# Optimization experiments

Hardware: AMD Instinct MI355X
Metric: run time of the kernel (lower is better)

Reference implementation:

```python
import jax, jax.numpy as jnp
import numpy as np

B, TOPK, E, C, K = 64, 2, 16, 1024, 4096


def setup_inputs() -> dict:
    key = jax.random.key(0)
    k1, k2, k3, k4, k5, k6 = jax.random.split(key, 6)
    return {
        "activated": jax.random.normal(k1, (B, TOPK, K), dtype=jnp.float32),
        "expert_indices": jax.random.randint(k2, (B, TOPK), 0, E, dtype=jnp.int64)
        if jax.config.jax_enable_x64 else jax.random.randint(k2, (B, TOPK), 0, E, dtype=jnp.int32),
        "expert_weights": jax.random.uniform(k3, (B, TOPK), dtype=jnp.float32),
        "mlp2_weight": jax.random.normal(k4, (E, C, K), dtype=jnp.float32),
        "mlp2_bias": jax.random.normal(k5, (E, C), dtype=jnp.float32),
        "residual_x": jax.random.normal(k6, (B, C), dtype=jnp.float32),
    }


def reference(activated, expert_indices, expert_weights, mlp2_weight, mlp2_bias, residual_x):
    # Gather per-token expert weights/biases: w [B, topk, C, K], b [B, topk, C]
    w = mlp2_weight[expert_indices]
    b = mlp2_bias[expert_indices]
    # Batched matvec per (token, expert slot): t [B, topk, C]
    t = jnp.einsum("beck,bek->bec", w, activated) + b
    # Weighted combine over top-k expert slots, plus residual: [B, C]
    return residual_x + jnp.einsum("bec,be->bc", t, expert_weights)
```

## Files before the change

### kernel.cpp

```cpp
#include <hip/hip_runtime.h>

#define BB    64
#define TOPK  2
#define EE    16
#define CC    1024
#define KK    4096

constexpr int RPB = 8;
constexpr int P   = 16;
constexpr int KC  = 512;
constexpr int KC4 = KC / 4;

__global__ __launch_bounds__(256) void route_init(
    const int* __restrict__ idx, const float* __restrict__ ew,
    const float* __restrict__ bias, const float* __restrict__ resid,
    float* __restrict__ out, int* __restrict__ cnt, int* __restrict__ lists)
{
    if (blockIdx.x == 0) {
        __shared__ int scnt[EE];
        if (threadIdx.x < EE) scnt[threadIdx.x] = 0;
        __syncthreads();
        if (threadIdx.x < BB * TOPK) {
            int e = idx[threadIdx.x];
            int pos = atomicAdd(&scnt[e], 1);
            lists[e * 128 + pos] = threadIdx.x;
        }
        __syncthreads();
        if (threadIdx.x < EE) cnt[threadIdx.x] = scnt[threadIdx.x];
    } else {
        int i = (blockIdx.x - 1) * 256 + threadIdx.x;
        int b = i >> 10;
        int c = i & (CC - 1);
        float v = resid[i];
#pragma unroll
        for (int s = 0; s < TOPK; s++) {
            int e = idx[b * TOPK + s];
            v += ew[b * TOPK + s] * bias[e * CC + c];
        }
        out[i] = v;
    }
}

__global__ __launch_bounds__(256, 2) void moe_mlp2(
    const float* __restrict__ act, const float* __restrict__ ew,
    const float* __restrict__ W, float* __restrict__ out,
    const int* __restrict__ cnt, const int* __restrict__ lists)
{
    __shared__ float sact[P][KC];
    __shared__ int   spair[P];

    const int e = blockIdx.x >> 7;
    const int n = cnt[e];
    if (n == 0) return;
    const int c0   = (blockIdx.x & 127) * RPB;
    const int tid  = threadIdx.x;
    const int lane = tid & 63;
    const int wave = tid >> 6;
    const float* We = W + (size_t)(e * CC + c0 + wave * 2) * KK;

    for (int g = 0; g < n; g += P) {
        const int np = min(P, n - g);
        if (tid < np) spair[tid] = lists[e * 128 + g + tid];
        __syncthreads();

        float acc[2][P];
#pragma unroll
        for (int r = 0; r < 2; r++)
#pragma unroll
            for (int p = 0; p < P; p++) acc[r][p] = 0.f;

        for (int kc = 0; kc < KK; kc += KC) {
            if (kc) __syncthreads();
            for (int t = tid; t < np * KC4; t += 256) {
                int p  = t >> 7;
                int kk = (t & (KC4 - 1)) << 2;
                *(float4*)&sact[p][kk] =
                    *(const float4*)(act + (size_t)spair[p] * KK + kc + kk);
            }
            __syncthreads();
#pragma unroll
            for (int ii = 0; ii < KC4 / 64; ii++) {
                int i = lane + ii * 64;
                float4 w4[2];
#pragma unroll
                for (int r = 0; r < 2; r++)
                    w4[r] = *(const float4*)(We + (size_t)r * KK + kc + 4 * i);
#pragma unroll
                for (int p = 0; p < P; p++) {
                    float4 a4 = *(const float4*)&sact[p][4 * i];
#pragma unroll
                    for (int r = 0; r < 2; r++)
                        acc[r][p] += w4[r].x * a4.x + w4[r].y * a4.y +
                                     w4[r].z * a4.z + w4[r].w * a4.w;
                }
            }
        }

#pragma unroll
        for (int r = 0; r < 2; r++) {
#pragma unroll
            for (int p = 0; p < P; p++) {
                if (p < np) {
                    float v = acc[r][p];
#pragma unroll
                    for (int off = 32; off > 0; off >>= 1)
                        v += __shfl_down(v, off, 64);
                    if (lane == 0) {
                        int pr = spair[p];
                        atomicAdd(out + (pr >> 1) * CC + c0 + wave * 2 + r,
                                  ew[pr] * v);
                    }
                }
            }
        }
        __syncthreads();
    }
}

extern "C" void kernel_launch(void* const* d_in, const int* in_sizes, int n_in,
                              void* d_out, int out_size, void* d_ws, size_t ws_size,
                              hipStream_t stream) {
    const float* act   = (const float*)d_in[0];
    const int*   idx   = (const int*)d_in[1];
    const float* ew    = (const float*)d_in[2];
    const float* W     = (const float*)d_in[3];
    const float* bias  = (const float*)d_in[4];
    const float* resid = (const float*)d_in[5];
    float* out = (float*)d_out;

    int* cnt   = (int*)d_ws;
    int* lists = (int*)d_ws + 64;

    route_init<<<1 + (BB * CC) / 256, 256, 0, stream>>>(
        idx, ew, bias, resid, out, cnt, lists);
    moe_mlp2<<<EE * (CC / RPB), 256, 0, stream>>>(
        act, ew, W, out, cnt, lists);
}
```

Before: 433.1 us.

## Read activations directly from global memory instead of staging through LDS

Removes the shared-memory staging of activation chunks and the block-wide barriers around it. Each lane now loads activation float4s straight from global memory using per-pair byte offsets held in registers, and the K loop becomes a single pass in groups of four pairs. The intent is to drop LDS traffic and syncthreads so the weight stream runs uninterrupted, relying on L2/L1 to serve the activation reuse across waves. The risk is more global/cache load traffic and higher register pressure, especially since the launch-bounds occupancy hint was also removed.

```diff
diff --git a/kernel.cpp b/kernel.cpp
--- a/kernel.cpp
+++ b/kernel.cpp
@@ -8,8 +8,7 @@
 
 constexpr int RPB = 8;
 constexpr int P   = 16;
-constexpr int KC  = 512;
-constexpr int KC4 = KC / 4;
+constexpr int NW  = KK / 4 / 64;
 
 __global__ __launch_bounds__(256) void route_init(
     const int* __restrict__ idx, const float* __restrict__ ew,
@@ -41,27 +40,27 @@
     }
 }
 
-__global__ __launch_bounds__(256, 2) void moe_mlp2(
+__global__ __launch_bounds__(256) void moe_mlp2(
     const float* __restrict__ act, const float* __restrict__ ew,
     const float* __restrict__ W, float* __restrict__ out,
     const int* __restrict__ cnt, const int* __restrict__ lists)
 {
-    __shared__ float sact[P][KC];
-    __shared__ int   spair[P];
-
     const int e = blockIdx.x >> 7;
     const int n = cnt[e];
     if (n == 0) return;
     const int c0   = (blockIdx.x & 127) * RPB;
-    const int tid  = threadIdx.x;
-    const int lane = tid & 63;
-    const int wave = tid >> 6;
-    const float* We = W + (size_t)(e * CC + c0 + wave * 2) * KK;
+    const int lane = threadIdx.x & 63;
+    const int wave = threadIdx.x >> 6;
+    const float4* We0 = (const float4*)(W + (size_t)(e * CC + c0 + wave * 2) * KK);
+    const float4* We1 = We0 + (KK / 4);
 
     for (int g = 0; g < n; g += P) {
         const int np = min(P, n - g);
-        if (tid < np) spair[tid] = lists[e * 128 + g + tid];
-        __syncthreads();
+
+        int aoff[P];
+#pragma unroll
+        for (int p = 0; p < P; p++)
+            aoff[p] = (p < np) ? lists[e * 128 + g + p] * (KK * 4) : 0;
 
         float acc[2][P];
 #pragma unroll
@@ -69,51 +68,45 @@
 #pragma unroll
             for (int p = 0; p < P; p++) acc[r][p] = 0.f;
 
-        for (int kc = 0; kc < KK; kc += KC) {
-            if (kc) __syncthreads();
-            for (int t = tid; t < np * KC4; t += 256) {
-                int p  = t >> 7;
-                int kk = (t & (KC4 - 1)) << 2;
-                *(float4*)&sact[p][kk] =
-                    *(const float4*)(act + (size_t)spair[p] * KK + kc + kk);
-            }
-            __syncthreads();
+#pragma unroll 2
+        for (int kw = 0; kw < NW; kw++) {
+            const int fi = kw * 64 + lane;
+            const float4 w0 = We0[fi];
+            const float4 w1 = We1[fi];
+            const char* abase = (const char*)act + ((size_t)fi << 4);
 #pragma unroll
-            for (int ii = 0; ii < KC4 / 64; ii++) {
-                int i = lane + ii * 64;
-                float4 w4[2];
+            for (int pc = 0; pc < P / 4; pc++) {
+                if (pc * 4 < np) {
 #pragma unroll
-                for (int r = 0; r < 2; r++)
-                    w4[r] = *(const float4*)(We + (size_t)r * KK + kc + 4 * i);
-#pragma unroll
-                for (int p = 0; p < P; p++) {
-                    float4 a4 = *(const float4*)&sact[p][4 * i];
-#pragma unroll
-                    for (int r = 0; r < 2; r++)
-                        acc[r][p] += w4[r].x * a4.x + w4[r].y * a4.y +
-                                     w4[r].z * a4.z + w4[r].w * a4.w;
+                    for (int j = 0; j < 4; j++) {
+                        const int p = pc * 4 + j;
+                        const float4 a = *(const float4*)(abase + aoff[p]);
+                        acc[0][p] += w0.x * a.x + w0.y * a.y + w0.z * a.z + w0.w * a.w;
+                        acc[1][p] += w1.x * a.x + w1.y * a.y + w1.z * a.z + w1.w * a.w;
+                    }
                 }
             }
         }
 
 #pragma unroll
-        for (int r = 0; r < 2; r++) {
+        for (int p = 0; p < P; p++) {
+            if (p < np) {
+                float v0 = acc[0][p];
+                float v1 = acc[1][p];
 #pragma unroll
-            for (int p = 0; p < P; p++) {
-                if (p < np) {
-                    float v = acc[r][p];
-#pragma unroll
-                    for (int off = 32; off > 0; off >>= 1)
-                        v += __shfl_down(v, off, 64);
-                    if (lane == 0) {
-                        int pr = spair[p];
-                        atomicAdd(out + (pr >> 1) * CC + c0 + wave * 2 + r,
-                                  ew[pr] * v);
-                    }
+                for (int off = 32; off > 0; off >>= 1) {
+                    v0 += __shfl_down(v0, off, 64);
+                    v1 += __shfl_down(v1, off, 64);
+                }
+                if (lane == 0) {
+                    int pr = lists[e * 128 + g + p];
+                    float w = ew[pr];
+                    float* o = out + (pr >> 1) * CC + c0 + wave * 2;
+                    atomicAdd(o + 0, w * v0);
+                    atomicAdd(o + 1, w * v1);
                 }
             }
         }
-        __syncthreads();
     }
 }
 
```

After: 404.6 us. -6.6%, faster.
